# Kernel optimization log

Hardware: AMD Instinct MI355X
Metric: run time of the kernel (lower is better)

The kernel has to match this reference:

```python
import jax, jax.numpy as jnp
import numpy as np
from jax import lax

A_RATIOS = (0.5, 1.0, 2.0)
A_SCALES = (8, 16, 32)
FEAT_STRIDE = 16
BASE_SIZE = 16
PRE_NMS = 6000     # n_test_pre_nms
POST_NMS = 300     # n_test_post_nms
NMS_THRESH = 0.7
MIN_SIZE = 16.0
SCALE = 1.0        # forward(scale=1.0) default
NEG = -1e10


def _anchor_base():
    # standard generate_anchor_base: centered at (8,8), ratios x scales
    py = px = BASE_SIZE / 2.0
    rows = []
    for r in A_RATIOS:
        for s in A_SCALES:
            h = BASE_SIZE * s * np.sqrt(r)
            w = BASE_SIZE * s * np.sqrt(1.0 / r)
            rows.append([py - h / 2.0, px - w / 2.0, py + h / 2.0, px + w / 2.0])
    return np.asarray(rows, np.float32)  # (A, 4)


def _all_anchors(height, width):
    base = jnp.asarray(_anchor_base())                                  # (A, 4)
    sy = (jnp.arange(height) * FEAT_STRIDE).astype(jnp.float32)
    sx = (jnp.arange(width) * FEAT_STRIDE).astype(jnp.float32)
    gy, gx = jnp.meshgrid(sy, sx, indexing='ij')
    shift = jnp.stack([gy.ravel(), gx.ravel(), gy.ravel(), gx.ravel()], axis=1)  # (K, 4)
    anch = base[None, :, :] + shift[:, None, :]                         # (K, A, 4)
    return anch.reshape(-1, 4)                                          # (K*A, 4)


def _conv(x, w, b, pad):
    y = lax.conv_general_dilated(x, w, (1, 1), [(pad, pad), (pad, pad)],
                                 dimension_numbers=('NCHW', 'OIHW', 'NCHW'))
    return y + b[None, :, None, None]


def _loc2bbox(anchors, locs):
    h = anchors[:, 2] - anchors[:, 0]
    w = anchors[:, 3] - anchors[:, 1]
    cy = anchors[:, 0] + 0.5 * h
    cx = anchors[:, 1] + 0.5 * w
    dy, dx, dh, dw = locs[:, 0], locs[:, 1], locs[:, 2], locs[:, 3]
    ncy = dy * h + cy
    ncx = dx * w + cx
    nh = jnp.exp(dh) * h
    nw = jnp.exp(dw) * w
    return jnp.stack([ncy - 0.5 * nh, ncx - 0.5 * nw,
                      ncy + 0.5 * nh, ncx + 0.5 * nw], axis=1)


def _iou_one_vs_all(box, boxes):
    ty = jnp.maximum(box[0], boxes[:, 0])
    tx = jnp.maximum(box[1], boxes[:, 1])
    by = jnp.minimum(box[2], boxes[:, 2])
    bx = jnp.minimum(box[3], boxes[:, 3])
    inter = jnp.maximum(by - ty, 0.0) * jnp.maximum(bx - tx, 0.0)
    a1 = (box[2] - box[0]) * (box[3] - box[1])
    a2 = (boxes[:, 2] - boxes[:, 0]) * (boxes[:, 3] - boxes[:, 1])
    return inter / (a1 + a2 - inter + 1e-9)


def _nms(boxes, scores):
    # greedy NMS with fixed POST_NMS output; invalid slots are zero boxes
    def step(s, _):
        i = jnp.argmax(s)
        valid = s[i] > NEG / 2
        ious = _iou_one_vs_all(boxes[i], boxes)
        s = jnp.where(ious > NMS_THRESH, NEG, s)  # suppresses self (iou=1)
        return s, (i, valid)
    _, (idx, valid) = lax.scan(step, scores, None, length=POST_NMS)
    return boxes[idx] * valid[:, None].astype(boxes.dtype)  # (POST_NMS, 4)


def _proposals(anchors, locs, fg, img_h, img_w):
    boxes = _loc2bbox(anchors, locs)
    boxes = jnp.stack([jnp.clip(boxes[:, 0], 0.0, img_h),
                       jnp.clip(boxes[:, 1], 0.0, img_w),
                       jnp.clip(boxes[:, 2], 0.0, img_h),
                       jnp.clip(boxes[:, 3], 0.0, img_w)], axis=1)
    hs = boxes[:, 2] - boxes[:, 0]
    ws = boxes[:, 3] - boxes[:, 1]
    ok = (hs >= MIN_SIZE * SCALE) & (ws >= MIN_SIZE * SCALE)
    sc = jnp.where(ok, fg, NEG)
    top_sc, idx = lax.top_k(sc, PRE_NMS)
    return _nms(boxes[idx], top_sc)


def reference(base_feat, W_conv1, b_conv1, W_score, b_score, W_loc, b_loc, img_h, img_w):
    N, _, H, W = base_feat.shape
    A = 9
    mid = jax.nn.relu(_conv(base_feat, W_conv1, b_conv1, 1))            # (N,512,H,W)
    rpn_locs = _conv(mid, W_loc, b_loc, 0).transpose(0, 2, 3, 1).reshape(N, H * W * A, 4)
    raw = _conv(mid, W_score, b_score, 0).transpose(0, 2, 3, 1)          # (N,H,W,2A)
    rpn_scores = raw.reshape(N, H * W * A, 2)
    fg = jax.nn.softmax(raw.reshape(N, H, W, A, 2), axis=-1)[..., 1].reshape(N, -1)
    anchors = _all_anchors(H, W)                                         # (H*W*A,4)
    ih, iw = float(img_h), float(img_w)
    prop = jax.vmap(lambda l, f: _proposals(anchors, l, f, ih, iw))(rpn_locs, fg)
    rois = prop.reshape(N * POST_NMS, 4)
    roi_indices = jnp.repeat(jnp.arange(N, dtype=jnp.int32), POST_NMS)
    return rpn_locs, rpn_scores, rois, roi_indices, anchors


def setup_inputs() -> dict:
    key = jax.random.key(0)
    k0, k1, k2, k3 = jax.random.split(key, 4)
    N, C, H, W = 4, 512, 64, 64
    nA = 9
    return {
        'base_feat': jax.random.normal(k0, (N, C, H, W), jnp.float32),
        'W_conv1': 0.01 * jax.random.normal(k1, (512, 512, 3, 3), jnp.float32),
        'b_conv1': jnp.zeros((512,), jnp.float32),
        'W_score': 0.01 * jax.random.normal(k2, (2 * nA, 512, 1, 1), jnp.float32),
        'b_score': jnp.zeros((2 * nA,), jnp.float32),
        'W_loc': 0.01 * jax.random.normal(k3, (4 * nA, 512, 1, 1), jnp.float32),
        'b_loc': jnp.zeros((4 * nA,), jnp.float32),
        'img_h': 1024,
        'img_w': 1024,
    }
```

## Files before the change

kernel.cpp:

```cpp
#include <hip/hip_runtime.h>
#include <math.h>

#define HH 64
#define WW 64
#define NIMG 4
#define CIN 512
#define AA 9
#define HWA (HH*WW*AA)
#define PRE_NMS 6000
#define POST_NMS 300
#define NEGV (-1e10f)
#define NEGK 0xD01502F9u
#define NWORD 94

#define OFF1 589824
#define OFF2 884736
#define OFF3 889536
#define OFF4 890736

typedef unsigned int u32;
typedef unsigned long long u64;
typedef _Float16 f16;
typedef _Float16 half8 __attribute__((ext_vector_type(8)));
typedef float f32x4 __attribute__((ext_vector_type(4)));

struct AnchBase { float v[36]; };

__device__ __forceinline__ void gload_lds16(const void* g, void* l)
{
    __builtin_amdgcn_global_load_lds((const __attribute__((address_space(1))) void*)g,
                                     (__attribute__((address_space(3))) void*)l,
                                     16, 0, 0);
}

__global__ __launch_bounds__(256) void k_prep_x(const float* __restrict__ x,
                                                f16* __restrict__ xh,
                                                f16* __restrict__ xl)
{
    __shared__ float tile[64][65];
    int ci0 = blockIdx.x * 64, y = blockIdx.y, n = blockIdx.z;
    int t = threadIdx.x;
    #pragma unroll
    for (int l = 0; l < 16; ++l) {
        int idx = l * 256 + t;
        int cc = idx >> 6, xc = idx & 63;
        tile[cc][xc] = x[((size_t)(n * CIN + ci0 + cc) * HH + y) * WW + xc];
    }
    __syncthreads();
    #pragma unroll
    for (int l = 0; l < 16; ++l) {
        int idx = l * 256 + t;
        int xc = idx >> 6, cc = idx & 63;
        float v = tile[cc][xc];
        f16 hi = (f16)v;
        f16 lo = (f16)(v - (float)hi);
        size_t o = ((size_t)(n * 64 + y) * 64 + xc) * 512 + ci0 + cc;
        xh[o] = hi; xl[o] = lo;
    }
}

__global__ __launch_bounds__(256) void k_prep_w(const float* __restrict__ W1,
                                                f16* __restrict__ wh,
                                                f16* __restrict__ wl)
{
    int idx = blockIdx.x * 256 + threadIdx.x;
    int co = idx >> 9, ci = idx & 511;
    #pragma unroll
    for (int tap = 0; tap < 9; ++tap) {
        float v = W1[(size_t)idx * 9 + tap];
        f16 hi = (f16)v;
        f16 lo = (f16)(v - (float)hi);
        size_t o = ((size_t)tap * 512 + co) * 512 + ci;
        wh[o] = hi; wl[o] = lo;
    }
}

__global__ __launch_bounds__(256, 4) void k_conv_mfma(const f16* __restrict__ xh,
                                                      const f16* __restrict__ xl,
                                                      const f16* __restrict__ wh,
                                                      const f16* __restrict__ wl,
                                                      const float* __restrict__ bias,
                                                      float* __restrict__ mid)
{
    __shared__ f16 sX[2][4][66][32];
    const int t = threadIdx.x;
    const int lid = blockIdx.x + 8 * (blockIdx.y + 32 * blockIdx.z);
    const int logical = (lid & 7) * 128 + (lid >> 3);
    const int co0 = (logical & 7) * 64;
    const int g = logical >> 3;
    const int yb = g & 31, n = g >> 5;
    const int y0 = yb * 2;
    const int wv = t >> 6, lane = t & 63;
    const int q = lane >> 4, li = lane & 15;
    const int mh = wv & 1;
    const int xhp = wv >> 1;

    {
        int pr = t >> 5, j = t & 31;
        int col = (j < 16) ? 0 : 65, e = j & 15;
        u32* p = (u32*)&sX[0][0][0][0];
        p[(pr >> 2) * 4224 + (pr & 3) * 1056 + col * 16 + e] = 0;
    }
    if (yb == 0 || yb == 31) {
        int r = (yb == 0) ? 0 : 3;
        u32* p = (u32*)&sX[0][0][0][0];
        #pragma unroll
        for (int l = 0; l < 9; ++l) {
            int idx = l * 256 + t;
            if (idx < 2112) {
                int plane = (idx >= 1056) ? 1 : 0;
                int rr = idx - plane * 1056;
                p[plane * 4224 + r * 1056 + rr] = 0;
            }
        }
    }

    f32x4 acc[2][2][2];
    #pragma unroll
    for (int mt = 0; mt < 2; ++mt)
        #pragma unroll
        for (int xn = 0; xn < 2; ++xn)
            #pragma unroll
            for (int yy = 0; yy < 2; ++yy)
                acc[mt][xn][yy] = (f32x4){0.f, 0.f, 0.f, 0.f};

    auto prefetch = [&](int ci0) {
        #pragma unroll
        for (int m = 0; m < 8; ++m) {
            int k2 = wv * 8 + m;
            int plane = k2 >> 4;
            int row = (k2 >> 2) & 3;
            int gy = y0 - 1 + row;
            if ((unsigned)gy < 64u) {
                int col = ((k2 & 3) << 4) + (lane >> 2);
                int s = (lane & 3) ^ ((lane >> 3) & 3);
                const f16* src = (plane ? xl : xh) +
                    (((size_t)(n * 64 + gy) * 64 + col) * 512 + ci0 + s * 8);
                f16* dst = &sX[0][0][0][0] + (size_t)plane * 8448 + row * 2112
                           + (1 + (k2 & 3) * 16) * 32 + lane * 8;
                gload_lds16(src, dst);
            }
        }
    };

    const size_t wb0 = (size_t)(co0 + mh * 32 + li) * 512 + q * 8;
    const f16* pWh = wh + wb0;
    const f16* pWl = wl + wb0;
    half8 wa[2][2], wn[2][2];
    auto loadW = [&](half8 (&w)[2][2], int ci0, int tap) {
        #pragma unroll
        for (int mt = 0; mt < 2; ++mt) {
            size_t off = (size_t)tap * 262144 + (size_t)mt * 8192 + ci0;
            w[0][mt] = *(const half8*)(pWh + off);
            w[1][mt] = *(const half8*)(pWl + off);
        }
    };

    const f16* pB[2][3];
    #pragma unroll
    for (int xn = 0; xn < 2; ++xn)
        #pragma unroll
        for (int kx = 0; kx < 3; ++kx) {
            int lc = xhp * 32 + xn * 16 + li + kx;
            int qe = q ^ (((lc - 1) >> 1) & 3);
            pB[xn][kx] = &sX[0][0][0][0] + lc * 32 + qe * 8;
        }

    auto loadB = [&](half8 (&Bf)[2][2][2], int tap) {
        const int ky = tap / 3, kx = tap - ky * 3;
        #pragma unroll
        for (int xn = 0; xn < 2; ++xn) {
            const f16* pb = pB[xn][kx];
            #pragma unroll
            for (int yy = 0; yy < 2; ++yy) {
                const f16* ph = pb + (yy + ky) * 2112;
                Bf[0][xn][yy] = *(const half8*)ph;
                Bf[1][xn][yy] = *(const half8*)(ph + 8448);
            }
        }
    };

    prefetch(0);
    loadW(wa, 0, 0);

    for (int chunk = 0; chunk < 16; ++chunk) {
        const int ci0 = chunk * 32;
        __syncthreads();

        half8 B0[2][2][2], Bn[2][2][2];
        loadB(B0, 0);

        #pragma unroll
        for (int tap = 0; tap < 9; ++tap) {
            if (tap < 8) {
                loadW(wn, ci0, tap + 1);
                loadB(Bn, tap + 1);
            }
            #pragma unroll
            for (int mt = 0; mt < 2; ++mt)
                #pragma unroll
                for (int xn = 0; xn < 2; ++xn)
                    #pragma unroll
                    for (int yy = 0; yy < 2; ++yy)
                        acc[mt][xn][yy] = __builtin_amdgcn_mfma_f32_16x16x32_f16(wa[0][mt], B0[0][xn][yy], acc[mt][xn][yy], 0, 0, 0);
            #pragma unroll
            for (int mt = 0; mt < 2; ++mt)
                #pragma unroll
                for (int xn = 0; xn < 2; ++xn)
                    #pragma unroll
                    for (int yy = 0; yy < 2; ++yy)
                        acc[mt][xn][yy] = __builtin_amdgcn_mfma_f32_16x16x32_f16(wa[0][mt], B0[1][xn][yy], acc[mt][xn][yy], 0, 0, 0);
            #pragma unroll
            for (int mt = 0; mt < 2; ++mt)
                #pragma unroll
                for (int xn = 0; xn < 2; ++xn)
                    #pragma unroll
                    for (int yy = 0; yy < 2; ++yy)
                        acc[mt][xn][yy] = __builtin_amdgcn_mfma_f32_16x16x32_f16(wa[1][mt], B0[0][xn][yy], acc[mt][xn][yy], 0, 0, 0);

            if (tap < 8) {
                #pragma unroll
                for (int pl = 0; pl < 2; ++pl)
                    #pragma unroll
                    for (int mt = 0; mt < 2; ++mt) wa[pl][mt] = wn[pl][mt];
                #pragma unroll
                for (int pl = 0; pl < 2; ++pl)
                    #pragma unroll
                    for (int xn = 0; xn < 2; ++xn)
                        #pragma unroll
                        for (int yy = 0; yy < 2; ++yy) B0[pl][xn][yy] = Bn[pl][xn][yy];
            }
        }

        if (chunk + 1 < 16) {
            __syncthreads();
            prefetch(ci0 + 32);
            loadW(wa, ci0 + 32, 0);
        }
    }

    #pragma unroll
    for (int mt = 0; mt < 2; ++mt) {
        #pragma unroll
        for (int r = 0; r < 4; ++r) {
            int co = co0 + mh * 32 + mt * 16 + q * 4 + r;
            float bv = bias[co];
            #pragma unroll
            for (int xn = 0; xn < 2; ++xn) {
                int xc = xhp * 32 + xn * 16 + li;
                #pragma unroll
                for (int yy = 0; yy < 2; ++yy) {
                    float v = acc[mt][xn][yy][r] + bv;
                    mid[((size_t)(n * 512 + co) * HH + y0 + yy) * WW + xc] = v > 0.f ? v : 0.f;
                }
            }
        }
    }
}

__global__ __launch_bounds__(256) void k_htrans(const float* __restrict__ Ws,
                                                const float* __restrict__ Wl,
                                                float* __restrict__ Wt2)
{
    int i = blockIdx.x * 256 + threadIdx.x;
    if (i >= 512 * 64) return;
    int ci = i >> 6, co = i & 63;
    float v = 0.f;
    if (co < 18) v = Ws[co * 512 + ci];
    else if (co < 54) v = Wl[(co - 18) * 512 + ci];
    Wt2[i] = v;
}

__global__ __launch_bounds__(256) void k_hgemm(const float* __restrict__ mid,
                                               const float* __restrict__ Wt2,
                                               float* __restrict__ sraw)
{
    __shared__ float sM[32][64];
    __shared__ float sW2[32][64];
    const int t = threadIdx.x;
    const int px0 = blockIdx.x * 64, n = blockIdx.y;
    const int tx = t & 15, ty = t >> 4;

    float acc[4][4];
    #pragma unroll
    for (int c = 0; c < 4; ++c)
        #pragma unroll
        for (int j = 0; j < 4; ++j) acc[c][j] = 0.f;

    for (int ci0 = 0; ci0 < 512; ci0 += 32) {
        __syncthreads();
        #pragma unroll
        for (int l = 0; l < 8; ++l) {
            int i = l * 256 + t;
            int ci = i >> 6, px = i & 63;
            sM[ci][px] = mid[((size_t)n * 512 + ci0 + ci) * 4096 + px0 + px];
            sW2[ci][px] = Wt2[(size_t)(ci0 + ci) * 64 + px];
        }
        __syncthreads();
        #pragma unroll
        for (int ci = 0; ci < 32; ++ci) {
            float mv[4], wv[4];
            #pragma unroll
            for (int j = 0; j < 4; ++j) mv[j] = sM[ci][tx * 4 + j];
            #pragma unroll
            for (int c = 0; c < 4; ++c) wv[c] = sW2[ci][ty * 4 + c];
            #pragma unroll
            for (int c = 0; c < 4; ++c)
                #pragma unroll
                for (int j = 0; j < 4; ++j) acc[c][j] += wv[c] * mv[j];
        }
    }
    #pragma unroll
    for (int c = 0; c < 4; ++c) {
        float4 v = make_float4(acc[c][0], acc[c][1], acc[c][2], acc[c][3]);
        *(float4*)&sraw[((size_t)n * 64 + ty * 4 + c) * 4096 + px0 + tx * 4] = v;
    }
}

__global__ __launch_bounds__(256) void k_decode(const float* __restrict__ sraw,
                                                const float* __restrict__ bsc,
                                                const float* __restrict__ blc,
                                                const int* __restrict__ ph,
                                                const int* __restrict__ pw,
                                                float* __restrict__ out,
                                                float* __restrict__ boxes,
                                                u32* __restrict__ key,
                                                AnchBase ab)
{
    int p = blockIdx.x * 256 + threadIdx.x;
    int n = p >> 12, pi = p & 4095;
    int y = pi >> 6, xq = pi & 63;

    const float* S = sraw + (size_t)n * 64 * 4096 + pi;
    float* o0 = out + (size_t)n * 147456;
    float* o1 = out + OFF1 + (size_t)n * 73728;
    float IHf = (float)(*ph), IWf = (float)(*pw);

    #pragma unroll
    for (int a = 0; a < 9; ++a) {
        float s0 = S[(size_t)(2 * a) * 4096] + bsc[2 * a];
        float s1 = S[(size_t)(2 * a + 1) * 4096] + bsc[2 * a + 1];
        float dy = S[(size_t)(18 + 4 * a) * 4096] + blc[4 * a];
        float dx = S[(size_t)(19 + 4 * a) * 4096] + blc[4 * a + 1];
        float dh = S[(size_t)(20 + 4 * a) * 4096] + blc[4 * a + 2];
        float dw = S[(size_t)(21 + 4 * a) * 4096] + blc[4 * a + 3];

        o1[(pi * 9 + a) * 2 + 0] = s0;
        o1[(pi * 9 + a) * 2 + 1] = s1;
        o0[(pi * 9 + a) * 4 + 0] = dy;
        o0[(pi * 9 + a) * 4 + 1] = dx;
        o0[(pi * 9 + a) * 4 + 2] = dh;
        o0[(pi * 9 + a) * 4 + 3] = dw;

        float mm = fmaxf(s0, s1);
        float e0 = expf(s0 - mm), e1 = expf(s1 - mm);
        float fg = e1 / (e0 + e1);

        float a0 = ab.v[4 * a + 0] + (float)(y * 16);
        float a1 = ab.v[4 * a + 1] + (float)(xq * 16);
        float a2 = ab.v[4 * a + 2] + (float)(y * 16);
        float a3 = ab.v[4 * a + 3] + (float)(xq * 16);

        float h = a2 - a0, w = a3 - a1;
        float cy = a0 + 0.5f * h, cx = a1 + 0.5f * w;
        float ncy = dy * h + cy, ncx = dx * w + cx;
        float nh = expf(dh) * h, nw = expf(dw) * w;
        float b0 = fminf(fmaxf(ncy - 0.5f * nh, 0.f), IHf);
        float b1 = fminf(fmaxf(ncx - 0.5f * nw, 0.f), IWf);
        float b2 = fminf(fmaxf(ncy + 0.5f * nh, 0.f), IHf);
        float b3 = fminf(fmaxf(ncx + 0.5f * nw, 0.f), IWf);

        bool ok = (b2 - b0 >= 16.0f) && (b3 - b1 >= 16.0f);
        float sc = ok ? fg : NEGV;

        int gi = n * HWA + pi * 9 + a;
        ((float4*)boxes)[gi] = make_float4(b0, b1, b2, b3);
        u32 u = __float_as_uint(sc);
        u32 kasc = (u & 0x80000000u) ? ~u : (u | 0x80000000u);
        key[gi] = ~kasc;
    }
}

__global__ void k_misc(float* __restrict__ out, AnchBase ab)
{
    int i = blockIdx.x * 256 + threadIdx.x;
    if (i < 4800) out[OFF2 + i] = 0.f;
    if (i < 1200) out[OFF3 + i] = (float)(i / 300);
    if (i < HWA) {
        int pi = i / 9, a = i - pi * 9;
        int y = pi >> 6, xq = pi & 63;
        out[OFF4 + i * 4 + 0] = ab.v[4 * a + 0] + (float)(y * 16);
        out[OFF4 + i * 4 + 1] = ab.v[4 * a + 1] + (float)(xq * 16);
        out[OFF4 + i * 4 + 2] = ab.v[4 * a + 2] + (float)(y * 16);
        out[OFF4 + i * 4 + 3] = ab.v[4 * a + 3] + (float)(xq * 16);
    }
}

__global__ __launch_bounds__(1024) void k_selsort(const u32* __restrict__ key,
                                                  const float* __restrict__ boxes,
                                                  float* __restrict__ boxesS,
                                                  int* __restrict__ nvalid)
{
    __shared__ u64 sK[8192];
    __shared__ int hist[256];
    __shared__ u32 sPref;
    __shared__ int sR;
    __shared__ int cLess, cEq, cVal;
    int n = blockIdx.x, t = threadIdx.x;
    const u32* k0 = key + (size_t)n * HWA;

    u32 pref = 0, mask = 0;
    int R = PRE_NMS;
    for (int pass = 0; pass < 4; ++pass) {
        int shift = 24 - pass * 8;
        if (t < 256) hist[t] = 0;
        __syncthreads();
        for (int i = t; i < HWA; i += 1024) {
            u32 k = k0[i];
            if ((k & mask) == pref) atomicAdd(&hist[(k >> shift) & 255], 1);
        }
        __syncthreads();
        if (t == 0) {
            int cum = 0;
            for (int b = 0; b < 256; ++b) {
                int c = hist[b];
                if (cum + c >= R) { sPref = pref | ((u32)b << shift); sR = R - cum; break; }
                cum += c;
            }
        }
        __syncthreads();
        pref = sPref; R = sR; mask |= (0xFFu << shift);
        __syncthreads();
    }
    u32 T = pref;
    if (t == 0) { cLess = 0; cEq = 0; cVal = 0; }
    __syncthreads();
    for (int i = t; i < HWA; i += 1024) {
        u32 k = k0[i];
        if (k < NEGK) atomicAdd(&cVal, 1);
        if (k < T) {
            int p = atomicAdd(&cLess, 1);
            sK[p] = ((u64)k << 32) | (u32)i;
        } else if (k == T) {
            int p = atomicAdd(&cEq, 1);
            if (p < R) sK[PRE_NMS - 1 - p] = ((u64)k << 32) | (u32)i;
        }
    }
    for (int i = PRE_NMS + t; i < 8192; i += 1024) sK[i] = ~0ull;
    __syncthreads();
    if (t == 0) nvalid[n] = cVal < PRE_NMS ? cVal : PRE_NMS;

    for (unsigned k = 2; k <= 8192; k <<= 1) {
        for (unsigned j = k >> 1; j > 0; j >>= 1) {
            __syncthreads();
            #pragma unroll
            for (int v = 0; v < 8; ++v) {
                int i = v * 1024 + t;
                int ixj = i ^ (int)j;
                if (ixj > i) {
                    u64 a = sK[i], b = sK[ixj];
                    bool up = ((i & (int)k) == 0);
                    if (up ? (a > b) : (a < b)) { sK[i] = b; sK[ixj] = a; }
                }
            }
        }
    }
    __syncthreads();
    const float4* bsrc = (const float4*)boxes + (size_t)n * HWA;
    float4* bdst = (float4*)boxesS + (size_t)n * PRE_NMS;
    for (int i = t; i < PRE_NMS; i += 1024) {
        u32 idx = (u32)(sK[i] & 0xFFFFFFFFu);
        bdst[i] = bsrc[idx];
    }
}

__global__ __launch_bounds__(64) void k_iou(const float* __restrict__ boxesS,
                                            u64* __restrict__ mask)
{
    __shared__ float4 cb[64];
    int w = blockIdx.x, ic = blockIdx.y, n = blockIdx.z;
    if (w < ic) return;
    int t = threadIdx.x;
    const float4* B = (const float4*)boxesS + (size_t)n * PRE_NMS;
    int jc = w * 64 + t;
    cb[t] = (jc < PRE_NMS) ? B[jc] : make_float4(0.f, 0.f, 0.f, 0.f);
    __syncthreads();
    int i = ic * 64 + t;
    if (i >= PRE_NMS) return;
    float4 bb = B[i];
    float area1 = (bb.z - bb.x) * (bb.w - bb.y);
    u64 m = 0;
    #pragma unroll 8
    for (int j = 0; j < 64; ++j) {
        float4 o = cb[j];
        float ty_ = fmaxf(bb.x, o.x), tx_ = fmaxf(bb.y, o.y);
        float by_ = fminf(bb.z, o.z), bx_ = fminf(bb.w, o.w);
        float inter = fmaxf(by_ - ty_, 0.f) * fmaxf(bx_ - tx_, 0.f);
        float area2 = (o.z - o.x) * (o.w - o.y);
        float iou = inter / (area1 + area2 - inter + 1e-9f);
        if (iou > 0.7f) m |= (1ull << j);
    }
    mask[((size_t)n * PRE_NMS + i) * NWORD + w] = m;
}

__global__ __launch_bounds__(64) void k_nms3(const u64* __restrict__ mask,
                                             const int* __restrict__ nvalid,
                                             const float* __restrict__ boxesS,
                                             float* __restrict__ rois)
{
    int n = blockIdx.x, lane = threadIdx.x;
    int nv = nvalid[n];
    const u64* M = mask + (size_t)n * PRE_NMS * NWORD;
    const float4* B = (const float4*)boxesS + (size_t)n * PRE_NMS;

    auto vmask = [&](int w) -> u64 {
        int lo = w * 64;
        if (nv >= lo + 64) return ~0ull;
        if (nv <= lo) return 0ull;
        return (1ull << (nv - lo)) - 1ull;
    };
    u64 vm0 = vmask(lane);
    u64 vm1 = (lane < NWORD - 64) ? vmask(64 + lane) : 0ull;
    u64 rem0 = 0, rem1 = 0;

    int cnt = 0;
    while (cnt < POST_NMS) {
        u64 c0 = (~rem0) & vm0;
        u64 c1 = (~rem1) & vm1;
        int sel;
        u64 b0 = __ballot(c0 != 0);
        if (b0) {
            int l = __builtin_ctzll(b0);
            u64 w = __shfl(c0, l);
            sel = l * 64 + __builtin_ctzll(w);
        } else {
            u64 b1 = __ballot(c1 != 0);
            if (!b1) break;
            int l = __builtin_ctzll(b1);
            u64 w = __shfl(c1, l);
            sel = (64 + l) * 64 + __builtin_ctzll(w);
        }
        if (lane == 0) {
            float4 bb = B[sel];
            float* orow = rois + (size_t)(n * POST_NMS + cnt) * 4;
            orow[0] = bb.x; orow[1] = bb.y; orow[2] = bb.z; orow[3] = bb.w;
        }
        const u64* Mr = M + (size_t)sel * NWORD;
        rem0 |= Mr[lane];
        if (lane < NWORD - 64) rem1 |= Mr[64 + lane];
        cnt++;
    }
}

extern "C" void kernel_launch(void* const* d_in, const int* in_sizes, int n_in,
                              void* d_out, int out_size, void* d_ws, size_t ws_size,
                              hipStream_t stream)
{
    const float* x  = (const float*)d_in[0];
    const float* W1 = (const float*)d_in[1];
    const float* b1 = (const float*)d_in[2];
    const float* Ws = (const float*)d_in[3];
    const float* bs = (const float*)d_in[4];
    const float* Wl = (const float*)d_in[5];
    const float* bl = (const float*)d_in[6];
    const int* ih   = (const int*)d_in[7];
    const int* iw   = (const int*)d_in[8];
    float* out = (float*)d_out;
    char* ws = (char*)d_ws;

    f16*   Wh2    = (f16*)  (ws);
    f16*   Wl2    = (f16*)  (ws + 4718592);
    float* mid    = (float*)(ws + 9437184);
    f16*   xh     = (f16*)  (ws + 42991616);
    f16*   xl     = (f16*)  (ws + 59768832);
    float* boxes  = (float*)(ws + 42991616);
    u32*   key    = (u32*)  (ws + 45350912);
    float* boxesS = (float*)(ws + 46202880);
    int*   nval   = (int*)  (ws + 46586880);
    float* Wt2    = (float*)(ws);
    float* sraw   = (float*)(ws + 262144);
    u64*   iomask = (u64*)  (ws + 9437184);

    AnchBase ab;
    for (int a = 0; a < 9; ++a) {
        int ri = a / 3, si = a - ri * 3;
        double s = (double)(8 << si);
        double rr = (ri == 0) ? 0.5 : ((ri == 1) ? 1.0 : 2.0);
        double hh = 16.0 * s * sqrt(rr);
        double wd = 16.0 * s * sqrt(1.0 / rr);
        ab.v[a * 4 + 0] = (float)(8.0 - hh * 0.5);
        ab.v[a * 4 + 1] = (float)(8.0 - wd * 0.5);
        ab.v[a * 4 + 2] = (float)(8.0 + hh * 0.5);
        ab.v[a * 4 + 3] = (float)(8.0 + wd * 0.5);
    }

    k_prep_x<<<dim3(8, 64, 4), 256, 0, stream>>>(x, xh, xl);
    k_prep_w<<<1024, 256, 0, stream>>>(W1, Wh2, Wl2);
    k_conv_mfma<<<dim3(8, 32, 4), 256, 0, stream>>>(xh, xl, Wh2, Wl2, b1, mid);
    k_htrans<<<128, 256, 0, stream>>>(Ws, Wl, Wt2);
    k_hgemm<<<dim3(64, 4), 256, 0, stream>>>(mid, Wt2, sraw);
    k_decode<<<64, 256, 0, stream>>>(sraw, bs, bl, ih, iw, out, boxes, key, ab);
    k_misc<<<144, 256, 0, stream>>>(out, ab);
    k_selsort<<<4, 1024, 0, stream>>>(key, boxes, boxesS, nval);
    k_iou<<<dim3(NWORD, NWORD, NIMG), 64, 0, stream>>>(boxesS, iomask);
    k_nms3<<<NIMG, 64, 0, stream>>>(iomask, nval, boxesS, out + OFF2);
}
```

Baseline: 823.3 us.

## Batch NMS candidate mask-row loads into LDS windows of sixteen

The serial greedy NMS loop is restructured. Each pass speculatively picks the next 16 surviving candidates, prefetches all of their suppression-mask rows into LDS with async global-to-LDS loads, and then resolves them in order, testing each against the updated keep mask. This is meant to hide the per-iteration global-load latency that dominated the sequential selection loop. The cost is wasted loads for candidates that end up suppressed inside a window, extra ballot/shuffle work, and a 16KB LDS buffer.

```diff
diff --git a/kernel.cpp b/kernel.cpp
--- a/kernel.cpp
+++ b/kernel.cpp
@@ -12,6 +12,7 @@
 #define NEGV (-1e10f)
 #define NEGK 0xD01502F9u
 #define NWORD 94
+#define WNMS 16
 
 #define OFF1 589824
 #define OFF2 884736
@@ -508,6 +509,7 @@
                                              const float* __restrict__ boxesS,
                                              float* __restrict__ rois)
 {
+    __shared__ u64 rowbuf[WNMS][128];
     int n = blockIdx.x, lane = threadIdx.x;
     int nv = nvalid[n];
     const u64* M = mask + (size_t)n * PRE_NMS * NWORD;
@@ -519,36 +521,74 @@
         if (nv <= lo) return 0ull;
         return (1ull << (nv - lo)) - 1ull;
     };
-    u64 vm0 = vmask(lane);
-    u64 vm1 = (lane < NWORD - 64) ? vmask(64 + lane) : 0ull;
-    u64 rem0 = 0, rem1 = 0;
+    u64 c0 = vmask(lane);
+    u64 c1 = (lane < NWORD - 64) ? vmask(64 + lane) : 0ull;
+
+    auto firstbit = [&](u64 a0, u64 a1) -> int {
+        u64 b0 = __ballot(a0 != 0);
+        if (b0) {
+            int l = __builtin_ctzll(b0);
+            u64 w = __shfl(a0, l);
+            return l * 64 + __builtin_ctzll(w);
+        }
+        u64 b1 = __ballot(a1 != 0);
+        if (!b1) return -1;
+        int l = __builtin_ctzll(b1);
+        u64 w = __shfl(a1, l);
+        return (64 + l) * 64 + __builtin_ctzll(w);
+    };
+    auto clearbit = [&](u64& a0, u64& a1, int s) {
+        int ws = s >> 6, b = s & 63;
+        if (lane == ws) a0 &= ~(1ull << b);
+        if (lane + 64 == ws) a1 &= ~(1ull << b);
+    };
+    auto testbit = [&](u64 a0, u64 a1, int s) -> bool {
+        int ws = s >> 6, b = s & 63;
+        u64 w = (ws < 64) ? __shfl(a0, ws) : __shfl(a1, ws - 64);
+        return (w >> b) & 1ull;
+    };
 
     int cnt = 0;
     while (cnt < POST_NMS) {
-        u64 c0 = (~rem0) & vm0;
-        u64 c1 = (~rem1) & vm1;
-        int sel;
-        u64 b0 = __ballot(c0 != 0);
-        if (b0) {
-            int l = __builtin_ctzll(b0);
-            u64 w = __shfl(c0, l);
-            sel = l * 64 + __builtin_ctzll(w);
-        } else {
-            u64 b1 = __ballot(c1 != 0);
-            if (!b1) break;
-            int l = __builtin_ctzll(b1);
-            u64 w = __shfl(c1, l);
-            sel = (64 + l) * 64 + __builtin_ctzll(w);
-        }
-        if (lane == 0) {
-            float4 bb = B[sel];
-            float* orow = rois + (size_t)(n * POST_NMS + cnt) * 4;
-            orow[0] = bb.x; orow[1] = bb.y; orow[2] = bb.z; orow[3] = bb.w;
-        }
-        const u64* Mr = M + (size_t)sel * NWORD;
-        rem0 |= Mr[lane];
-        if (lane < NWORD - 64) rem1 |= Mr[64 + lane];
-        cnt++;
+        u64 t0 = c0, t1 = c1;
+        int widx[WNMS];
+        int wn = 0;
+        #pragma unroll
+        for (int k = 0; k < WNMS; ++k) {
+            int idx = firstbit(t0, t1);
+            widx[k] = idx;
+            if (idx >= 0) { clearbit(t0, t1, idx); wn = k + 1; }
+        }
+        if (wn == 0) break;
+
+        #pragma unroll
+        for (int k = 0; k < WNMS; ++k) {
+            if (k < wn) {
+                const char* src = (const char*)(M + (size_t)widx[k] * NWORD) + lane * 16;
+                gload_lds16(src, &rowbuf[k][0]);
+            }
+        }
+        asm volatile("s_waitcnt vmcnt(0)" ::: "memory");
+        __builtin_amdgcn_sched_barrier(0);
+
+        #pragma unroll
+        for (int k = 0; k < WNMS; ++k) {
+            if (k < wn && cnt < POST_NMS) {
+                int sel = widx[k];
+                if (testbit(c0, c1, sel)) {
+                    if (lane == 0) {
+                        float4 bb = B[sel];
+                        float* orow = rois + (size_t)(n * POST_NMS + cnt) * 4;
+                        orow[0] = bb.x; orow[1] = bb.y; orow[2] = bb.z; orow[3] = bb.w;
+                    }
+                    cnt++;
+                    u64 m0 = rowbuf[k][lane];
+                    u64 m1 = (lane < NWORD - 64) ? rowbuf[k][64 + lane] : 0ull;
+                    c0 &= ~m0; c1 &= ~m1;
+                    clearbit(c0, c1, sel);
+                }
+            }
+        }
     }
 }
 
```

Measured after the change: 819.2 us. Within noise of the previous version (-0.5%).

## Restructure NMS scan into per-chunk blocked resolution with LDS diagonal masks

Applied to the files above, without the earlier changes.

The serial NMS selection loop is replaced by a chunk-by-chunk scan. For each 64-box chunk, the diagonal mask words are prefetched into LDS and used to resolve suppression inside the chunk with shuffles. Mask rows for all boxes selected in that chunk are then loaded in batches of eight and applied to the remaining candidates. This removes the dependent global-load round trip on every selection and lets independent row loads overlap, at the cost of a large upfront LDS prefetch and more complex control flow.

```diff
diff --git a/kernel.cpp b/kernel.cpp
--- a/kernel.cpp
+++ b/kernel.cpp
@@ -508,6 +508,7 @@
                                              const float* __restrict__ boxesS,
                                              float* __restrict__ rois)
 {
+    __shared__ u64 diag[NWORD * 128];
     int n = blockIdx.x, lane = threadIdx.x;
     int nv = nvalid[n];
     const u64* M = mask + (size_t)n * PRE_NMS * NWORD;
@@ -519,36 +520,65 @@
         if (nv <= lo) return 0ull;
         return (1ull << (nv - lo)) - 1ull;
     };
-    u64 vm0 = vmask(lane);
-    u64 vm1 = (lane < NWORD - 64) ? vmask(64 + lane) : 0ull;
-    u64 rem0 = 0, rem1 = 0;
+    u64 c0 = vmask(lane);
+    u64 c1 = (lane < NWORD - 64) ? vmask(64 + lane) : 0ull;
+
+    for (int c = 0; c < NWORD; ++c) {
+        int i = c * 64 + lane;
+        if (i < PRE_NMS) {
+            const char* src = (const char*)(M + (size_t)i * NWORD + (c & ~1));
+            gload_lds16(src, &diag[(size_t)c * 128]);
+        }
+    }
+    asm volatile("s_waitcnt vmcnt(0)" ::: "memory");
+    __builtin_amdgcn_sched_barrier(0);
 
     int cnt = 0;
-    while (cnt < POST_NMS) {
-        u64 c0 = (~rem0) & vm0;
-        u64 c1 = (~rem1) & vm1;
-        int sel;
-        u64 b0 = __ballot(c0 != 0);
-        if (b0) {
-            int l = __builtin_ctzll(b0);
-            u64 w = __shfl(c0, l);
-            sel = l * 64 + __builtin_ctzll(w);
-        } else {
-            u64 b1 = __ballot(c1 != 0);
-            if (!b1) break;
-            int l = __builtin_ctzll(b1);
-            u64 w = __shfl(c1, l);
-            sel = (64 + l) * 64 + __builtin_ctzll(w);
-        }
-        if (lane == 0) {
-            float4 bb = B[sel];
-            float* orow = rois + (size_t)(n * POST_NMS + cnt) * 4;
-            orow[0] = bb.x; orow[1] = bb.y; orow[2] = bb.z; orow[3] = bb.w;
-        }
-        const u64* Mr = M + (size_t)sel * NWORD;
-        rem0 |= Mr[lane];
-        if (lane < NWORD - 64) rem1 |= Mr[64 + lane];
-        cnt++;
+    for (int c = 0; c < NWORD; ++c) {
+        u64 w = (c < 64) ? __shfl(c0, c) : __shfl(c1, c - 64);
+        if (w == 0) continue;
+
+        u64 dl = diag[(size_t)c * 128 + lane * 2 + (c & 1)];
+
+        u64 selw = 0;
+        u64 ww = w;
+        while (ww && cnt < POST_NMS) {
+            int j = __builtin_ctzll(ww);
+            int sel = c * 64 + j;
+            if (lane == 0) {
+                float4 bb = B[sel];
+                float* orow = rois + (size_t)(n * POST_NMS + cnt) * 4;
+                orow[0] = bb.x; orow[1] = bb.y; orow[2] = bb.z; orow[3] = bb.w;
+            }
+            cnt++;
+            selw |= 1ull << j;
+            u64 dj = __shfl(dl, j);
+            ww &= ~dj;
+            ww &= ~(1ull << j);
+        }
+        if (cnt >= POST_NMS) break;
+
+        u64 s = selw;
+        while (s) {
+            int ids[8];
+            u64 r0v[8], r1v[8];
+            #pragma unroll
+            for (int z = 0; z < 8; ++z) {
+                int idz = -1;
+                if (s) { int j = __builtin_ctzll(s); s &= s - 1; idz = c * 64 + j; }
+                ids[z] = idz;
+            }
+            #pragma unroll
+            for (int z = 0; z < 8; ++z) {
+                if (ids[z] >= 0) {
+                    const u64* Mr = M + (size_t)ids[z] * NWORD;
+                    r0v[z] = Mr[lane];
+                    r1v[z] = (lane < NWORD - 64) ? Mr[64 + lane] : 0ull;
+                } else { r0v[z] = 0ull; r1v[z] = 0ull; }
+            }
+            #pragma unroll
+            for (int z = 0; z < 8; ++z) { c0 &= ~r0v[z]; c1 &= ~r1v[z]; }
+        }
     }
 }
 
```

Result: faster. 775.3 us (-5.8%).
